# Kernel optimization log

Measured on AMD Instinct MI355X. Metric: run time of the kernel, lower is better.

## Reference

```python
import jax, jax.numpy as jnp
from jax import lax
import numpy as np


def _double_swish(x):
    # DoubleSwish(x) = x * sigmoid(x - 1)
    return x * jax.nn.sigmoid(x - 1.0)


def setup_inputs() -> dict:
    key = jax.random.key(0)
    ks = jax.random.split(key, 32)
    L, N, E, H, DFF, K = 1024, 4, 512, 8, 2048, 31
    d = E // (2 * H)  # head_dim = embed_dim // (num_heads * 2) = 32

    def g(i, shape, scale):
        return jax.random.normal(ks[i], shape, dtype=jnp.float32) * scale

    return {
        "src": g(0, (L, N, E), 1.0),
        "pos_emb": g(1, (1, 2 * L - 1, E), 1.0),
        "attn_scores_in": g(2, (N, L, L, H), 0.1),
        # attention params
        "w_in": g(3, (3 * E // 2, E), E ** -0.5),
        "b_in": g(4, (3 * E // 2,), 0.01),
        "w_pos": g(5, (E // 2, E), E ** -0.5),
        "pos_bias_u": g(6, (H, d), 0.05),
        "pos_bias_v": g(7, (H, d), 0.05),
        "proj_in": jnp.eye(H, dtype=jnp.float32) + g(8, (H, H), 0.1),
        "proj_out": g(9, (H, H), 0.1),
        "w_out": g(10, (E, E // 2), 0.05 * (E // 2) ** -0.5),  # ScaledLinear initial_scale=0.05
        "b_out": g(11, (E,), 0.01),
        # macaron FFN
        "w_ff1m": g(12, (DFF, E), E ** -0.5),
        "b_ff1m": g(13, (DFF,), 0.01),
        "w_ff2m": g(14, (E, DFF), 0.25 * DFF ** -0.5),
        "b_ff2m": g(15, (E,), 0.01),
        # final FFN
        "w_ff1": g(16, (DFF, E), E ** -0.5),
        "b_ff1": g(17, (DFF,), 0.01),
        "w_ff2": g(18, (E, DFF), 0.25 * DFF ** -0.5),
        "b_ff2": g(19, (E,), 0.01),
        # conv module
        "w_pw1": g(20, (2 * E, E), E ** -0.5),
        "b_pw1": g(21, (2 * E,), 0.01),
        "w_dw": g(22, (E, K), K ** -0.5),
        "b_dw": g(23, (E,), 0.01),
        "w_pw2": g(24, (E, E), 0.05 * E ** -0.5),  # ScaledConv1d initial_scale=0.05
        "b_pw2": g(25, (E,), 0.01),
        "norm_eps": jnp.array(0.25, dtype=jnp.float32),  # BasicNorm learned log-eps
    }


def reference(src, pos_emb, attn_scores_in, w_in, b_in, w_pos, pos_bias_u, pos_bias_v,
              proj_in, proj_out, w_out, b_out, w_ff1m, b_ff1m, w_ff2m, b_ff2m,
              w_ff1, b_ff1, w_ff2, b_ff2, w_pw1, b_pw1, w_dw, b_dw, w_pw2, b_pw2, norm_eps):
    L, N, E = src.shape
    H, d = pos_bias_u.shape
    K = w_dw.shape[1]

    def ff(x, w1, b1, w2, b2):
        return _double_swish(x @ w1.T + b1) @ w2.T + b2

    # macaron feed-forward (ActivationBalancer + dropout are identity at eval)
    x = src + ff(src, w_ff1m, b_ff1m, w_ff2m, b_ff2m)

    # --- rel-pos multi-head self-attention ---
    qkv = x @ w_in.T + b_in                          # (L,N,3E/2)
    q, k, v = jnp.split(qkv, 3, axis=-1)             # each (L,N,E/2)
    q = q.reshape(L, N, H, d).transpose(1, 2, 0, 3)  # (N,H,L,d)
    k = k.reshape(L, N, H, d).transpose(1, 2, 0, 3)
    v = v.reshape(L, N, H, d).transpose(1, 2, 0, 3)
    p = (pos_emb @ w_pos.T).reshape(2 * L - 1, H, d)  # (2L-1,H,d)

    ac = jnp.einsum('nhld,nhsd->nhls', q + pos_bias_u[None, :, None, :], k)
    bd = jnp.einsum('nhld,mhd->nhlm', q + pos_bias_v[None, :, None, :], p)  # (N,H,L,2L-1)
    # rel_shift: out[b,h,i,j] = bd[b,h,i,(L-1)-i+j]
    idx = (L - 1) - jnp.arange(L)[:, None] + jnp.arange(L)[None, :]  # (L,L)
    bd = jnp.take_along_axis(bd, idx[None, None], axis=-1)            # (N,H,L,L)

    scaling = d ** -0.5
    scores_in = jnp.einsum('nlsh,hg->ngls', attn_scores_in, proj_in)  # project then (N,H,L,L)
    total = (ac + bd) * scaling + scores_in
    attn = jax.nn.softmax(total, axis=-1)
    ctx = jnp.einsum('nhls,nhsd->nhld', attn, v)
    ctx = ctx.transpose(2, 0, 1, 3).reshape(L, N, E // 2)
    attn_out = ctx @ w_out.T + b_out
    scores_out = jnp.einsum('nhls,hg->nlsg', total, proj_out) + attn_scores_in
    x = x + attn_out

    # --- convolution module ---
    xc = x.transpose(1, 2, 0)                                        # (N,C,L)
    h = jnp.einsum('ncl,oc->nol', xc, w_pw1) + b_pw1[None, :, None]  # pointwise 1x1 -> 2C
    a, b = jnp.split(h, 2, axis=1)
    h = a * jax.nn.sigmoid(b)                                        # GLU(dim=1)
    pad = (K - 1) // 2
    h = lax.conv_general_dilated(h, w_dw[:, None, :], (1,), [(pad, pad)],
                                 feature_group_count=E,
                                 dimension_numbers=('NCH', 'OIH', 'NCH')) + b_dw[None, :, None]
    h = _double_swish(h)
    h = jnp.einsum('ncl,oc->nol', h, w_pw2) + b_pw2[None, :, None]
    x = x + h.transpose(2, 0, 1)

    # final feed-forward + BasicNorm
    x = x + ff(x, w_ff1, b_ff1, w_ff2, b_ff2)
    x = x * lax.rsqrt(jnp.mean(x * x, axis=-1, keepdims=True) + jnp.exp(norm_eps))
    return (x, scores_out)
```

## Files before the change

### kernel.cpp

```cpp
#include <hip/hip_runtime.h>

#define DEV_INLINE __device__ __forceinline__

typedef short bf16x8 __attribute__((ext_vector_type(8)));
typedef float f32x4 __attribute__((ext_vector_type(4)));
typedef unsigned short u16x8 __attribute__((ext_vector_type(8)));
typedef _Float16 f16x8 __attribute__((ext_vector_type(8)));
typedef _Float16 f16x2 __attribute__((ext_vector_type(2)));

DEV_INLINE float sigmoidf_(float x) { return 1.f / (1.f + __expf(-x)); }
DEV_INLINE unsigned short f2bf(float x) {
    unsigned int u = __float_as_uint(x);
    unsigned int r = (u + 0x7FFFu + ((u >> 16) & 1u)) >> 16;
    return (unsigned short)r;
}
DEV_INLINE float bf2f(unsigned short u) {
    return __uint_as_float(((unsigned int)u) << 16);
}
DEV_INLINE float fdot2_(f16x2 a, f16x2 b, float c) {
#if __has_builtin(__builtin_amdgcn_fdot2)
    return __builtin_amdgcn_fdot2(a, b, c, false);
#else
    return c + (float)a[0] * (float)b[0] + (float)a[1] * (float)b[1];
#endif
}
#define SL(v, k) __builtin_shufflevector(v, v, 2 * (k), 2 * (k) + 1)

struct CastJobs {
    const float4* src[11];
    ushort4* dst[11];
    int end[11];
};

__global__ __launch_bounds__(256) void cast_all_kernel(CastJobs jobs, int total4)
{
    int gi = blockIdx.x * 256 + threadIdx.x;
    if (gi >= total4) return;
    int s = 0, base = 0;
    while (gi >= jobs.end[s]) { base = jobs.end[s]; s++; }
    int li = gi - base;
    float4 v = jobs.src[s][li];
    ushort4 o = {f2bf(v.x), f2bf(v.y), f2bf(v.z), f2bf(v.w)};
    jobs.dst[s][li] = o;
}

template<int ACT, int RES, int WF32, int WBF>
__global__ __launch_bounds__(256) void mfma_gemm(
    const unsigned short* __restrict__ A, const unsigned short* __restrict__ B,
    const float* __restrict__ bias, const float* __restrict__ res,
    float* __restrict__ C, unsigned short* __restrict__ Cb, int M, int N, int K)
{
    __shared__ __align__(16) unsigned short As[128 * 32];
    __shared__ __align__(16) unsigned short Bs[128 * 32];

    const int t = threadIdx.x;
    const int lane = t & 63, wave = t >> 6;
    const int wr = wave >> 1, wc = wave & 1;
    const int lr = lane & 15, lk = lane >> 4;
    const int m0 = blockIdx.y * 128, n0 = blockIdx.x * 128;

    f32x4 acc[4][4] = {};

    for (int k0 = 0; k0 < K; k0 += 32) {
#pragma unroll
        for (int c = 0; c < 2; c++) {
            int bo = t * 16 + c * 4096;
            int row = bo >> 6;
            int col = (bo & 63) >> 1;
            __builtin_amdgcn_global_load_lds(
                (const __attribute__((address_space(1))) void*)(A + (size_t)(m0 + row) * K + k0 + col),
                (__attribute__((address_space(3))) void*)(As + (bo >> 1)), 16, 0, 0);
            __builtin_amdgcn_global_load_lds(
                (const __attribute__((address_space(1))) void*)(B + (size_t)(n0 + row) * K + k0 + col),
                (__attribute__((address_space(3))) void*)(Bs + (bo >> 1)), 16, 0, 0);
        }
        __syncthreads();

        bf16x8 af[4], bfr[4];
#pragma unroll
        for (int mi = 0; mi < 4; mi++)
            af[mi] = *(const bf16x8*)(As + (wr * 64 + mi * 16 + lr) * 32 + lk * 8);
#pragma unroll
        for (int nj = 0; nj < 4; nj++)
            bfr[nj] = *(const bf16x8*)(Bs + (wc * 64 + nj * 16 + lr) * 32 + lk * 8);
#pragma unroll
        for (int mi = 0; mi < 4; mi++)
#pragma unroll
            for (int nj = 0; nj < 4; nj++)
                acc[mi][nj] = __builtin_amdgcn_mfma_f32_16x16x32_bf16(
                    af[mi], bfr[nj], acc[mi][nj], 0, 0, 0);
        __syncthreads();
    }

#pragma unroll
    for (int nj = 0; nj < 4; nj++) {
        int col = n0 + wc * 64 + nj * 16 + lr;
        float bv = bias ? bias[col] : 0.f;
#pragma unroll
        for (int mi = 0; mi < 4; mi++) {
            int row = m0 + wr * 64 + mi * 16 + lk * 4;
#pragma unroll
            for (int j = 0; j < 4; j++) {
                int r = row + j;
                if (r >= M) continue;
                float v = acc[mi][nj][j] + bv;
                if (ACT) v = v * sigmoidf_(v - 1.f);
                size_t off = (size_t)r * N + col;
                if (RES) v += res[off];
                if (WF32) C[off] = v;
                if (WBF) Cb[off] = f2bf(v);
            }
        }
    }
}

template<int ACT, int RES, int WF32, int WBF>
__global__ __launch_bounds__(256) void mfma_gemm_n64(
    const unsigned short* __restrict__ A, const unsigned short* __restrict__ B,
    const float* __restrict__ bias, const float* __restrict__ res,
    float* __restrict__ C, unsigned short* __restrict__ Cb, int M, int N, int K)
{
    __shared__ __align__(16) unsigned short As[128 * 32];
    __shared__ __align__(16) unsigned short Bs[64 * 32];

    const int t = threadIdx.x;
    const int lane = t & 63, wave = t >> 6;
    const int wr = wave >> 1, wc = wave & 1;
    const int lr = lane & 15, lk = lane >> 4;
    const int m0 = blockIdx.y * 128, n0 = blockIdx.x * 64;

    f32x4 acc[4][2] = {};

    for (int k0 = 0; k0 < K; k0 += 32) {
#pragma unroll
        for (int c = 0; c < 2; c++) {
            int bo = t * 16 + c * 4096;
            int row = bo >> 6;
            int col = (bo & 63) >> 1;
            __builtin_amdgcn_global_load_lds(
                (const __attribute__((address_space(1))) void*)(A + (size_t)(m0 + row) * K + k0 + col),
                (__attribute__((address_space(3))) void*)(As + (bo >> 1)), 16, 0, 0);
        }
        {
            int bo = t * 16;
            int row = bo >> 6;
            int col = (bo & 63) >> 1;
            __builtin_amdgcn_global_load_lds(
                (const __attribute__((address_space(1))) void*)(B + (size_t)(n0 + row) * K + k0 + col),
                (__attribute__((address_space(3))) void*)(Bs + (bo >> 1)), 16, 0, 0);
        }
        __syncthreads();

        bf16x8 af[4], bfr[2];
#pragma unroll
        for (int mi = 0; mi < 4; mi++)
            af[mi] = *(const bf16x8*)(As + (wr * 64 + mi * 16 + lr) * 32 + lk * 8);
#pragma unroll
        for (int nj = 0; nj < 2; nj++)
            bfr[nj] = *(const bf16x8*)(Bs + (wc * 32 + nj * 16 + lr) * 32 + lk * 8);
#pragma unroll
        for (int mi = 0; mi < 4; mi++)
#pragma unroll
            for (int nj = 0; nj < 2; nj++)
                acc[mi][nj] = __builtin_amdgcn_mfma_f32_16x16x32_bf16(
                    af[mi], bfr[nj], acc[mi][nj], 0, 0, 0);
        __syncthreads();
    }

#pragma unroll
    for (int nj = 0; nj < 2; nj++) {
        int col = n0 + wc * 32 + nj * 16 + lr;
        float bv = bias ? bias[col] : 0.f;
#pragma unroll
        for (int mi = 0; mi < 4; mi++) {
            int row = m0 + wr * 64 + mi * 16 + lk * 4;
#pragma unroll
            for (int j = 0; j < 4; j++) {
                int r = row + j;
                float v = acc[mi][nj][j] + bv;
                if (ACT) v = v * sigmoidf_(v - 1.f);
                size_t off = (size_t)r * N + col;
                if (RES) v += res[off];
                if (WF32) C[off] = v;
                if (WBF) Cb[off] = f2bf(v);
            }
        }
    }
}

__global__ __launch_bounds__(256) void split_kernel(
    const float* __restrict__ qkv,
    const float* __restrict__ pbu, const float* __restrict__ pbv,
    _Float16* __restrict__ quh, _Float16* __restrict__ qvh,
    _Float16* __restrict__ kh, unsigned short* __restrict__ vt)
{
    int idx = blockIdx.x * 256 + threadIdx.x;
    int dd = idx & 31;
    int l  = (idx >> 5) & 1023;
    int nh = idx >> 15;
    int h  = nh & 7;
    int n  = nh >> 3;
    size_t base = ((size_t)l * 4 + n) * 768 + h * 32 + dd;
    float q = qkv[base];
    quh[idx] = (_Float16)(q + pbu[h * 32 + dd]);
    qvh[idx] = (_Float16)(q + pbv[h * 32 + dd]);
    kh[idx]  = (_Float16)qkv[base + 256];
    vt[(size_t)nh * 32768 + dd * 1024 + l] = f2bf(qkv[base + 512]);
}

__global__ __launch_bounds__(256) void repack_p_kernel(
    const float* __restrict__ pb, _Float16* __restrict__ p2h)
{
    int idx = blockIdx.x * 256 + threadIdx.x;
    if (idx >= 2047 * 256) return;
    int dd = idx & 31;
    int h  = (idx >> 5) & 7;
    int m  = idx >> 8;
    p2h[((size_t)h * 2047 + m) * 32 + dd] = (_Float16)pb[idx];
}

__global__ __launch_bounds__(256) void scores_kernel(
    const _Float16* __restrict__ quh, const _Float16* __restrict__ qvh,
    const _Float16* __restrict__ kh, const _Float16* __restrict__ p2h,
    unsigned short* __restrict__ totb)
{
    __shared__ __align__(16) float4 Qu4h[64 * 5];
    __shared__ __align__(16) float4 Qv4h[64 * 5];
    __shared__ __align__(16) float4 K4h[64 * 5];
    __shared__ __align__(16) float4 P4h[127 * 5 + 3];
    __shared__ __align__(16) unsigned short staged[64][72];

    const int t = threadIdx.x;
    const int tx = t & 15, ty = t >> 4;
    const int j0 = blockIdx.x * 64, i0 = blockIdx.y * 64;
    const int nh = blockIdx.z;
    const int h = nh & 7;
    const int m_base = 960 - i0 + j0;

    const float4* qug = (const float4*)(quh + ((size_t)nh * 1024 + i0) * 32);
    const float4* qvg = (const float4*)(qvh + ((size_t)nh * 1024 + i0) * 32);
    const float4* kg  = (const float4*)(kh + ((size_t)nh * 1024 + j0) * 32);
    const float4* pg  = (const float4*)(p2h + ((size_t)h * 2047 + m_base) * 32);

    {
        int r = t >> 2, c = t & 3;
        Qu4h[r * 5 + c] = qug[t];
        Qv4h[r * 5 + c] = qvg[t];
        K4h[r * 5 + c]  = kg[t];
    }
#pragma unroll
    for (int cc = 0; cc < 2; cc++) {
        int fi = t + 256 * cc;
        if (fi < 508) {
            int r = fi >> 2, c = fi & 3;
            P4h[r * 5 + c] = pg[fi];
        }
    }
    __syncthreads();

    float acc[4][4] = {};
    const int pbase = 63 + tx - ty;

#pragma unroll
    for (int dg = 0; dg < 4; dg++) {
        f16x8 qu_[4], qv_[4], k_[4], p_[7];
#pragma unroll
        for (int ii = 0; ii < 4; ii++) {
            qu_[ii] = __builtin_bit_cast(f16x8, Qu4h[(ty + 16 * ii) * 5 + dg]);
            qv_[ii] = __builtin_bit_cast(f16x8, Qv4h[(ty + 16 * ii) * 5 + dg]);
        }
#pragma unroll
        for (int jj = 0; jj < 4; jj++)
            k_[jj] = __builtin_bit_cast(f16x8, K4h[(tx + 16 * jj) * 5 + dg]);
#pragma unroll
        for (int s = 0; s < 7; s++)
            p_[s] = __builtin_bit_cast(f16x8, P4h[(pbase + 16 * (s - 3)) * 5 + dg]);
#pragma unroll
        for (int ii = 0; ii < 4; ii++)
#pragma unroll
            for (int jj = 0; jj < 4; jj++) {
                f16x8 a = qu_[ii], b = k_[jj];
                f16x8 av = qv_[ii], pv = p_[jj - ii + 3];
                float r = acc[ii][jj];
                r = fdot2_(SL(a, 0), SL(b, 0), r);
                r = fdot2_(SL(a, 1), SL(b, 1), r);
                r = fdot2_(SL(a, 2), SL(b, 2), r);
                r = fdot2_(SL(a, 3), SL(b, 3), r);
                r = fdot2_(SL(av, 0), SL(pv, 0), r);
                r = fdot2_(SL(av, 1), SL(pv, 1), r);
                r = fdot2_(SL(av, 2), SL(pv, 2), r);
                r = fdot2_(SL(av, 3), SL(pv, 3), r);
                acc[ii][jj] = r;
            }
    }

    const float scale = 0.17677669529663687f;
#pragma unroll
    for (int ii = 0; ii < 4; ii++)
#pragma unroll
        for (int jj = 0; jj < 4; jj++)
            staged[ty + 16 * ii][tx + 16 * jj] = f2bf(acc[ii][jj] * scale);
    __syncthreads();

    unsigned short* o = totb + ((size_t)nh * 1024 + i0) * 1024 + j0;
    int r = t >> 2, q = t & 3;
    u16x8 v0 = *(const u16x8*)&staged[r][q * 16];
    u16x8 v1 = *(const u16x8*)&staged[r][q * 16 + 8];
    *(u16x8*)(o + (size_t)r * 1024 + q * 16) = v0;
    *(u16x8*)(o + (size_t)r * 1024 + q * 16 + 8) = v1;
}

__global__ __launch_bounds__(512) void attn_finish_kernel(
    unsigned short* __restrict__ totb, const float* __restrict__ as_,
    const float* __restrict__ proj_in, const float* __restrict__ proj_out,
    float* __restrict__ out_s)
{
    __shared__ float pin_s[64], po_s[64];
    __shared__ float redbuf[8][8];

    const int t = threadIdx.x;
    const int n = blockIdx.x >> 10;
    const int i = blockIdx.x & 1023;
    const int j0 = t * 2;
    const int wave = t >> 6, lane = t & 63;

    if (t < 64) { pin_s[t] = proj_in[t]; po_s[t] = proj_out[t]; }
    __syncthreads();

    float th[8][2];
#pragma unroll
    for (int h = 0; h < 8; h++) {
        unsigned int u = *(const unsigned int*)(totb + ((size_t)(n * 8 + h) * 1024 + i) * 1024 + j0);
        th[h][0] = bf2f((unsigned short)(u & 0xffffu));
        th[h][1] = bf2f((unsigned short)(u >> 16));
    }

    const float4* as4 = (const float4*)(as_ + (((size_t)n * 1024 + i) * 1024 + j0) * 8);
    float4* os4 = (float4*)(out_s + (((size_t)n * 1024 + i) * 1024 + j0) * 8);

#pragma unroll
    for (int jj = 0; jj < 2; jj++) {
        float4 alo = as4[jj * 2];
        float4 ahi = as4[jj * 2 + 1];
        float ag[8] = {alo.x, alo.y, alo.z, alo.w, ahi.x, ahi.y, ahi.z, ahi.w};
#pragma unroll
        for (int h = 0; h < 8; h++) {
            float si = 0.f;
#pragma unroll
            for (int g = 0; g < 8; g++) si += ag[g] * pin_s[g * 8 + h];
            th[h][jj] += si;
        }
        float so[8];
#pragma unroll
        for (int g = 0; g < 8; g++) {
            float s = ag[g];
#pragma unroll
            for (int h = 0; h < 8; h++) s += th[h][jj] * po_s[h * 8 + g];
            so[g] = s;
        }
        float4 o0 = {so[0], so[1], so[2], so[3]};
        float4 o1 = {so[4], so[5], so[6], so[7]};
        os4[jj * 2] = o0;
        os4[jj * 2 + 1] = o1;
    }

    float sm[8];
#pragma unroll
    for (int h = 0; h < 8; h++) {
        th[h][0] = __expf(th[h][0]);
        th[h][1] = __expf(th[h][1]);
        sm[h] = th[h][0] + th[h][1];
    }
#pragma unroll
    for (int d = 1; d < 64; d <<= 1)
#pragma unroll
        for (int h = 0; h < 8; h++) sm[h] += __shfl_xor(sm[h], d);
    if (lane == 0)
#pragma unroll
        for (int h = 0; h < 8; h++) redbuf[wave][h] = sm[h];
    __syncthreads();

#pragma unroll
    for (int h = 0; h < 8; h++) {
        float s = 0.f;
#pragma unroll
        for (int w = 0; w < 8; w++) s += redbuf[w][h];
        float rs = 1.f / s;
        unsigned int lo = f2bf(th[h][0] * rs);
        unsigned int hi = f2bf(th[h][1] * rs);
        *(unsigned int*)(totb + ((size_t)(n * 8 + h) * 1024 + i) * 1024 + j0) =
            lo | (hi << 16);
    }
}

__global__ __launch_bounds__(256) void ctx_mfma_kernel(
    const unsigned short* __restrict__ attnb, const unsigned short* __restrict__ vt,
    unsigned short* __restrict__ ctx_b)
{
    __shared__ __align__(16) unsigned short As[128 * 32];
    __shared__ __align__(16) unsigned short Bs[32 * 32];

    const int t = threadIdx.x;
    const int lane = t & 63, wave = t >> 6;
    const int lr = lane & 15, lk = lane >> 4;
    const int i0 = blockIdx.x * 128;
    const int nh = blockIdx.y;
    const int n = nh >> 3, h = nh & 7;

    const unsigned short* Abase = attnb + ((size_t)nh * 1024 + i0) * 1024;
    const unsigned short* Bbase = vt + (size_t)nh * 32768;

    f32x4 acc[2][2] = {};

    for (int k0 = 0; k0 < 1024; k0 += 32) {
#pragma unroll
        for (int c = 0; c < 2; c++) {
            int bo = t * 16 + c * 4096;
            int row = bo >> 6;
            int col = (bo & 63) >> 1;
            __builtin_amdgcn_global_load_lds(
                (const __attribute__((address_space(1))) void*)(Abase + (size_t)row * 1024 + k0 + col),
                (__attribute__((address_space(3))) void*)(As + (bo >> 1)), 16, 0, 0);
        }
        if (t < 128) {
            int bo = t * 16;
            int row = bo >> 6;
            int col = (bo & 63) >> 1;
            __builtin_amdgcn_global_load_lds(
                (const __attribute__((address_space(1))) void*)(Bbase + (size_t)row * 1024 + k0 + col),
                (__attribute__((address_space(3))) void*)(Bs + (bo >> 1)), 16, 0, 0);
        }
        __syncthreads();

        bf16x8 af[2], bf_[2];
#pragma unroll
        for (int mi = 0; mi < 2; mi++)
            af[mi] = *(const bf16x8*)(As + (wave * 32 + mi * 16 + lr) * 32 + lk * 8);
#pragma unroll
        for (int nj = 0; nj < 2; nj++)
            bf_[nj] = *(const bf16x8*)(Bs + (nj * 16 + lr) * 32 + lk * 8);
#pragma unroll
        for (int mi = 0; mi < 2; mi++)
#pragma unroll
            for (int nj = 0; nj < 2; nj++)
                acc[mi][nj] = __builtin_amdgcn_mfma_f32_16x16x32_bf16(
                    af[mi], bf_[nj], acc[mi][nj], 0, 0, 0);
        __syncthreads();
    }

#pragma unroll
    for (int nj = 0; nj < 2; nj++) {
        int d = nj * 16 + lr;
#pragma unroll
        for (int mi = 0; mi < 2; mi++) {
            int ibase = i0 + wave * 32 + mi * 16 + lk * 4;
#pragma unroll
            for (int j = 0; j < 4; j++) {
                int i = ibase + j;
                ctx_b[((size_t)i * 4 + n) * 256 + h * 32 + d] = f2bf(acc[mi][nj][j]);
            }
        }
    }
}

__global__ __launch_bounds__(256) void glu_kernel(
    const unsigned short* __restrict__ h1, unsigned short* __restrict__ g)
{
    int idx4 = blockIdx.x * 256 + threadIdx.x;
    int r = idx4 >> 7, c4 = idx4 & 127;
    const ushort4* row = (const ushort4*)(h1 + (size_t)r * 1024);
    ushort4 a = row[c4];
    ushort4 b = row[128 + c4];
    ushort4 o = {f2bf(bf2f(a.x) * sigmoidf_(bf2f(b.x))),
                 f2bf(bf2f(a.y) * sigmoidf_(bf2f(b.y))),
                 f2bf(bf2f(a.z) * sigmoidf_(bf2f(b.z))),
                 f2bf(bf2f(a.w) * sigmoidf_(bf2f(b.w)))};
    ((ushort4*)g)[idx4] = o;
}

__global__ __launch_bounds__(256) void dwconv_kernel(
    const unsigned short* __restrict__ g, const float* __restrict__ w_dw,
    const float* __restrict__ b_dw, unsigned short* __restrict__ out)
{
    int idx = blockIdx.x * 256 + threadIdx.x;
    int c = idx & 511;
    int r = idx >> 9;
    int nn = r & 3, l = r >> 2;
    float acc = b_dw[c];
#pragma unroll
    for (int kk = 0; kk < 31; kk++) {
        int l2 = l + kk - 15;
        if (l2 >= 0 && l2 < 1024)
            acc += bf2f(g[(((size_t)l2 * 4 + nn) << 9) + c]) * w_dw[c * 31 + kk];
    }
    out[idx] = f2bf(acc * sigmoidf_(acc - 1.f));
}

__global__ __launch_bounds__(256) void norm_kernel(
    const float* __restrict__ x, const float* __restrict__ eps_p,
    float* __restrict__ out)
{
    int r = blockIdx.x, t = threadIdx.x;
    float a = x[(size_t)r * 512 + t];
    float b = x[(size_t)r * 512 + 256 + t];
    float ss = a * a + b * b;
#pragma unroll
    for (int d = 1; d < 64; d <<= 1) ss += __shfl_xor(ss, d);
    __shared__ float red[4];
    if ((t & 63) == 0) red[t >> 6] = ss;
    __syncthreads();
    float tot = red[0] + red[1] + red[2] + red[3];
    float scale = rsqrtf(tot * (1.f / 512.f) + __expf(eps_p[0]));
    out[(size_t)r * 512 + t] = a * scale;
    out[(size_t)r * 512 + 256 + t] = b * scale;
}

extern "C" void kernel_launch(void* const* d_in, const int* in_sizes, int n_in,
                              void* d_out, int out_size, void* d_ws, size_t ws_size,
                              hipStream_t stream)
{
    const float* src   = (const float*)d_in[0];
    const float* pos   = (const float*)d_in[1];
    const float* as_   = (const float*)d_in[2];
    const float* w_in  = (const float*)d_in[3];
    const float* b_in  = (const float*)d_in[4];
    const float* w_pos = (const float*)d_in[5];
    const float* pbu   = (const float*)d_in[6];
    const float* pbv   = (const float*)d_in[7];
    const float* prin  = (const float*)d_in[8];
    const float* prout = (const float*)d_in[9];
    const float* w_out = (const float*)d_in[10];
    const float* b_out = (const float*)d_in[11];
    const float* w_ff1m = (const float*)d_in[12];
    const float* b_ff1m = (const float*)d_in[13];
    const float* w_ff2m = (const float*)d_in[14];
    const float* b_ff2m = (const float*)d_in[15];
    const float* w_ff1 = (const float*)d_in[16];
    const float* b_ff1 = (const float*)d_in[17];
    const float* w_ff2 = (const float*)d_in[18];
    const float* b_ff2 = (const float*)d_in[19];
    const float* w_pw1 = (const float*)d_in[20];
    const float* b_pw1 = (const float*)d_in[21];
    const float* w_dw  = (const float*)d_in[22];
    const float* b_dw  = (const float*)d_in[23];
    const float* w_pw2 = (const float*)d_in[24];
    const float* b_pw2 = (const float*)d_in[25];
    const float* neps  = (const float*)d_in[26];

    float* out_x = (float*)d_out;
    float* out_s = (float*)d_out + 2097152;

    float* ws = (float*)d_ws;
    float* xbuf = ws;
    float* U    = xbuf + 2097152;
    float* sbbf = U + 6291456;
    float* xb16f= sbbf + 1048576;
    float* qkvb = xb16f + 1048576;
    float* qu   = qkvb + 3145728;
    float* qv   = qu + 1048576;
    float* kbuf = qv + 1048576;
    float* vbuf = kbuf + 1048576;
    float* pbuf = vbuf + 1048576;
    float* posbf= pbuf + 524288;
    float* totf = posbf + 524288;
    float* Wreg = totf + 16777216;

    unsigned short* hb16  = (unsigned short*)U;
    unsigned short* gbuf  = (unsigned short*)(U + 4194304);
    unsigned short* sbb   = (unsigned short*)sbbf;
    unsigned short* dbufb = (unsigned short*)sbbf;
    unsigned short* xb16  = (unsigned short*)xb16f;
    unsigned short* ctxb  = (unsigned short*)qu;
    unsigned short* posb  = (unsigned short*)posbf;
    unsigned short* totb  = (unsigned short*)totf;
    unsigned short* vt    = (unsigned short*)vbuf;
    _Float16*       quh   = (_Float16*)qu;
    _Float16*       qvh   = (_Float16*)qv;
    _Float16*       kh    = (_Float16*)kbuf;
    _Float16*       p2h   = (_Float16*)qkvb;

    float* wp = Wreg;
    unsigned short* wff1m_b = (unsigned short*)wp; wp += 524288;
    unsigned short* wff2m_b = (unsigned short*)wp; wp += 524288;
    unsigned short* win_b   = (unsigned short*)wp; wp += 196608;
    unsigned short* wpos_b  = (unsigned short*)wp; wp += 65536;
    unsigned short* wout_b  = (unsigned short*)wp; wp += 65536;
    unsigned short* wpw1_b  = (unsigned short*)wp; wp += 262144;
    unsigned short* wpw2_b  = (unsigned short*)wp; wp += 131072;
    unsigned short* wff1_b  = (unsigned short*)wp; wp += 524288;
    unsigned short* wff2_b  = (unsigned short*)wp; wp += 524288;

    dim3 blk(256);
    dim3 blk512(512);
    const int M = 4096;

    {
        CastJobs jobs;
        const float* srcs[11] = {src, pos, w_ff1m, w_ff2m, w_in, w_pos,
                                 w_out, w_pw1, w_pw2, w_ff1, w_ff2};
        unsigned short* dsts[11] = {sbb, posb, wff1m_b, wff2m_b, win_b, wpos_b,
                                    wout_b, wpw1_b, wpw2_b, wff1_b, wff2_b};
        int n4s[11] = {524288, 262016, 262144, 262144, 98304, 32768,
                       32768, 131072, 65536, 262144, 262144};
        int cum = 0;
        for (int s = 0; s < 11; s++) {
            jobs.src[s] = (const float4*)srcs[s];
            jobs.dst[s] = (ushort4*)dsts[s];
            cum += n4s[s];
            jobs.end[s] = cum;
        }
        cast_all_kernel<<<(cum + 255) / 256, blk, 0, stream>>>(jobs, cum);
    }

    mfma_gemm<1,0,0,1><<<dim3(16, 32), blk, 0, stream>>>(
        sbb, wff1m_b, b_ff1m, nullptr, nullptr, hb16, M, 2048, 512);
    mfma_gemm_n64<0,1,1,1><<<dim3(8, 32), blk, 0, stream>>>(
        hb16, wff2m_b, b_ff2m, src, xbuf, xb16, M, 512, 2048);

    mfma_gemm_n64<0,0,1,0><<<dim3(12, 32), blk, 0, stream>>>(
        xb16, win_b, b_in, nullptr, qkvb, nullptr, M, 768, 512);
    split_kernel<<<4096, blk, 0, stream>>>(qkvb, pbu, pbv, quh, qvh, kh, vt);
    mfma_gemm<0,0,1,0><<<dim3(2, 16), blk, 0, stream>>>(
        posb, wpos_b, nullptr, nullptr, pbuf, nullptr, 2047, 256, 512);
    repack_p_kernel<<<2047, blk, 0, stream>>>(pbuf, p2h);
    scores_kernel<<<dim3(16, 16, 32), blk, 0, stream>>>(quh, qvh, kh, p2h, totb);
    attn_finish_kernel<<<4096, blk512, 0, stream>>>(totb, as_, prin, prout, out_s);
    ctx_mfma_kernel<<<dim3(8, 32), blk, 0, stream>>>(totb, vt, ctxb);
    mfma_gemm_n64<0,1,1,1><<<dim3(8, 32), blk, 0, stream>>>(
        ctxb, wout_b, b_out, xbuf, xbuf, xb16, M, 512, 256);

    mfma_gemm<0,0,0,1><<<dim3(8, 32), blk, 0, stream>>>(
        xb16, wpw1_b, b_pw1, nullptr, nullptr, hb16, M, 1024, 512);
    glu_kernel<<<2048, blk, 0, stream>>>(hb16, gbuf);
    dwconv_kernel<<<8192, blk, 0, stream>>>(gbuf, w_dw, b_dw, dbufb);
    mfma_gemm_n64<0,1,1,1><<<dim3(8, 32), blk, 0, stream>>>(
        dbufb, wpw2_b, b_pw2, xbuf, xbuf, xb16, M, 512, 512);

    mfma_gemm<1,0,0,1><<<dim3(16, 32), blk, 0, stream>>>(
        xb16, wff1_b, b_ff1, nullptr, nullptr, hb16, M, 2048, 512);
    mfma_gemm_n64<0,1,1,0><<<dim3(8, 32), blk, 0, stream>>>(
        hb16, wff2_b, b_ff2, xbuf, xbuf, nullptr, M, 512, 2048);
    norm_kernel<<<4096, blk, 0, stream>>>(xbuf, neps, out_x);
}
```

Baseline: 522.8 us.

## Interleave heads in attention score buffer and widen per-thread work in softmax

Changes the bf16 attention score buffer layout from [n,h,i,j] to [n,i,h,j], so the finish kernel's eight head rows for a given query sit in one contiguous 16 KB span. The scores and ctx kernels are updated to use the new addressing. The finish kernel now runs 256 threads that each handle four columns with 8-byte loads and stores, which halves the cross-wave reduction. The aim is better locality and fewer, wider memory transactions in the memory-bound finish kernel. The cost is more register pressure and more strided row access in the ctx GEMM's A loads.

```diff
diff --git a/kernel.cpp b/kernel.cpp
--- a/kernel.cpp
+++ b/kernel.cpp
@@ -234,7 +234,7 @@
     const int tx = t & 15, ty = t >> 4;
     const int j0 = blockIdx.x * 64, i0 = blockIdx.y * 64;
     const int nh = blockIdx.z;
-    const int h = nh & 7;
+    const int n = nh >> 3, h = nh & 7;
     const int m_base = 960 - i0 + j0;
 
     const float4* qug = (const float4*)(quh + ((size_t)nh * 1024 + i0) * 32);
@@ -302,44 +302,46 @@
             staged[ty + 16 * ii][tx + 16 * jj] = f2bf(acc[ii][jj] * scale);
     __syncthreads();
 
-    unsigned short* o = totb + ((size_t)nh * 1024 + i0) * 1024 + j0;
     int r = t >> 2, q = t & 3;
+    unsigned short* o = totb + (((size_t)(n * 1024 + i0 + r)) * 8 + h) * 1024 + j0;
     u16x8 v0 = *(const u16x8*)&staged[r][q * 16];
     u16x8 v1 = *(const u16x8*)&staged[r][q * 16 + 8];
-    *(u16x8*)(o + (size_t)r * 1024 + q * 16) = v0;
-    *(u16x8*)(o + (size_t)r * 1024 + q * 16 + 8) = v1;
-}
-
-__global__ __launch_bounds__(512) void attn_finish_kernel(
+    *(u16x8*)(o + q * 16) = v0;
+    *(u16x8*)(o + q * 16 + 8) = v1;
+}
+
+__global__ __launch_bounds__(256) void attn_finish_kernel(
     unsigned short* __restrict__ totb, const float* __restrict__ as_,
     const float* __restrict__ proj_in, const float* __restrict__ proj_out,
     float* __restrict__ out_s)
 {
     __shared__ float pin_s[64], po_s[64];
-    __shared__ float redbuf[8][8];
+    __shared__ float redbuf[4][8];
 
     const int t = threadIdx.x;
     const int n = blockIdx.x >> 10;
     const int i = blockIdx.x & 1023;
-    const int j0 = t * 2;
+    const int j0 = t * 4;
     const int wave = t >> 6, lane = t & 63;
 
     if (t < 64) { pin_s[t] = proj_in[t]; po_s[t] = proj_out[t]; }
     __syncthreads();
 
-    float th[8][2];
+    unsigned short* tbase = totb + ((size_t)(n * 1024 + i)) * 8192;
+
+    float th[8][4];
 #pragma unroll
     for (int h = 0; h < 8; h++) {
-        unsigned int u = *(const unsigned int*)(totb + ((size_t)(n * 8 + h) * 1024 + i) * 1024 + j0);
-        th[h][0] = bf2f((unsigned short)(u & 0xffffu));
-        th[h][1] = bf2f((unsigned short)(u >> 16));
+        ushort4 u = *(const ushort4*)(tbase + h * 1024 + j0);
+        th[h][0] = bf2f(u.x); th[h][1] = bf2f(u.y);
+        th[h][2] = bf2f(u.z); th[h][3] = bf2f(u.w);
     }
 
     const float4* as4 = (const float4*)(as_ + (((size_t)n * 1024 + i) * 1024 + j0) * 8);
     float4* os4 = (float4*)(out_s + (((size_t)n * 1024 + i) * 1024 + j0) * 8);
 
 #pragma unroll
-    for (int jj = 0; jj < 2; jj++) {
+    for (int jj = 0; jj < 4; jj++) {
         float4 alo = as4[jj * 2];
         float4 ahi = as4[jj * 2 + 1];
         float ag[8] = {alo.x, alo.y, alo.z, alo.w, ahi.x, ahi.y, ahi.z, ahi.w};
@@ -367,9 +369,13 @@
     float sm[8];
 #pragma unroll
     for (int h = 0; h < 8; h++) {
-        th[h][0] = __expf(th[h][0]);
-        th[h][1] = __expf(th[h][1]);
-        sm[h] = th[h][0] + th[h][1];
+        float s = 0.f;
+#pragma unroll
+        for (int jj = 0; jj < 4; jj++) {
+            th[h][jj] = __expf(th[h][jj]);
+            s += th[h][jj];
+        }
+        sm[h] = s;
     }
 #pragma unroll
     for (int d = 1; d < 64; d <<= 1)
@@ -382,14 +388,10 @@
 
 #pragma unroll
     for (int h = 0; h < 8; h++) {
-        float s = 0.f;
-#pragma unroll
-        for (int w = 0; w < 8; w++) s += redbuf[w][h];
-        float rs = 1.f / s;
-        unsigned int lo = f2bf(th[h][0] * rs);
-        unsigned int hi = f2bf(th[h][1] * rs);
-        *(unsigned int*)(totb + ((size_t)(n * 8 + h) * 1024 + i) * 1024 + j0) =
-            lo | (hi << 16);
+        float rs = 1.f / (redbuf[0][h] + redbuf[1][h] + redbuf[2][h] + redbuf[3][h]);
+        ushort4 o = {f2bf(th[h][0] * rs), f2bf(th[h][1] * rs),
+                     f2bf(th[h][2] * rs), f2bf(th[h][3] * rs)};
+        *(ushort4*)(tbase + h * 1024 + j0) = o;
     }
 }
 
@@ -407,7 +409,6 @@
     const int nh = blockIdx.y;
     const int n = nh >> 3, h = nh & 7;
 
-    const unsigned short* Abase = attnb + ((size_t)nh * 1024 + i0) * 1024;
     const unsigned short* Bbase = vt + (size_t)nh * 32768;
 
     f32x4 acc[2][2] = {};
@@ -419,7 +420,8 @@
             int row = bo >> 6;
             int col = (bo & 63) >> 1;
             __builtin_amdgcn_global_load_lds(
-                (const __attribute__((address_space(1))) void*)(Abase + (size_t)row * 1024 + k0 + col),
+                (const __attribute__((address_space(1))) void*)(
+                    attnb + (((size_t)(n * 1024 + i0 + row)) * 8 + h) * 1024 + k0 + col),
                 (__attribute__((address_space(3))) void*)(As + (bo >> 1)), 16, 0, 0);
         }
         if (t < 128) {
@@ -591,7 +593,6 @@
     unsigned short* wff2_b  = (unsigned short*)wp; wp += 524288;
 
     dim3 blk(256);
-    dim3 blk512(512);
     const int M = 4096;
 
     {
@@ -624,7 +625,7 @@
         posb, wpos_b, nullptr, nullptr, pbuf, nullptr, 2047, 256, 512);
     repack_p_kernel<<<2047, blk, 0, stream>>>(pbuf, p2h);
     scores_kernel<<<dim3(16, 16, 32), blk, 0, stream>>>(quh, qvh, kh, p2h, totb);
-    attn_finish_kernel<<<4096, blk512, 0, stream>>>(totb, as_, prin, prout, out_s);
+    attn_finish_kernel<<<4096, blk, 0, stream>>>(totb, as_, prin, prout, out_s);
     ctx_mfma_kernel<<<dim3(8, 32), blk, 0, stream>>>(totb, vt, ctxb);
     mfma_gemm_n64<0,1,1,1><<<dim3(8, 32), blk, 0, stream>>>(
         ctxb, wout_b, b_out, xbuf, xbuf, xb16, M, 512, 256);
```

After: 510.5 us. -2.4%, faster.
